# Optimization experiments

Hardware: AMD Instinct MI355X
Metric: run time of the kernel (lower is better)

## Reference

```python
import jax, jax.numpy as jnp
import numpy as np

ANGULAR = 5
N_LAYERS = 3
H = 384
W = 384
N = 1
RANK = 4
C = 3


def make_filters(angular, n_layers, h, w):
    """Replicates the buffer built in multilayer.__init__: shape [n_layers, angular^2, h, w, 2]."""
    x = np.linspace(-1.0, 1.0, w)
    y = np.linspace(-1.0, 1.0, h)
    xv, yv = np.meshgrid(x, y)
    default_flow = np.stack([xv, yv], axis=-1)  # [h, w, 2]
    disp = np.zeros((angular ** 2, h, w, 2))
    a = 0
    for k in range(-angular // 2 + 1, angular // 2 + 1):
        for l in range(-angular // 2 + 1, angular // 2 + 1):
            disp[a, :, :, 0] = (-1.0 / w) * l
            disp[a, :, :, 1] = (-1.0 / h) * k
            a += 1
    layers = np.stack([disp * c for c in range(-n_layers // 2 + 1, n_layers // 2 + 1)], 0)
    layers += default_flow[None, None, ...]
    return jnp.asarray(layers, dtype=jnp.float32)


def setup_inputs() -> dict:
    key = jax.random.key(0)
    layers = jax.random.normal(key, (N, N_LAYERS, RANK, C, H, W), dtype=jnp.float32)
    filters = make_filters(ANGULAR, N_LAYERS, H, W)
    return {"layers": layers, "filters": filters}


def _warp(img, grid):
    """Bilinear grid_sample, padding_mode='border', align_corners=True.
    img: [N, H, W, C] channel-last; grid: [H, W, 2] normalized coords in [-1, 1].
    Returns [N, H, W, C]."""
    h, w = img.shape[1], img.shape[2]
    # unnormalize with align_corners=True, then border-clamp the coordinate
    x = jnp.clip((grid[..., 0] + 1.0) * 0.5 * (w - 1), 0.0, w - 1.0)
    y = jnp.clip((grid[..., 1] + 1.0) * 0.5 * (h - 1), 0.0, h - 1.0)
    x0 = jnp.floor(x)
    y0 = jnp.floor(y)
    wx = (x - x0)[..., None]  # [H, W, 1]
    wy = (y - y0)[..., None]
    x0i = x0.astype(jnp.int32)
    y0i = y0.astype(jnp.int32)
    x1i = jnp.minimum(x0i + 1, w - 1)
    y1i = jnp.minimum(y0i + 1, h - 1)
    v00 = img[:, y0i, x0i]  # [N, H, W, C]
    v01 = img[:, y0i, x1i]
    v10 = img[:, y1i, x0i]
    v11 = img[:, y1i, x1i]
    top = v00 + wx * (v01 - v00)
    bot = v10 + wx * (v11 - v10)
    return top + wy * (bot - top)


def _forward(layers, filters):
    n, num_layers, rank, c, h, w = layers.shape
    a2 = filters.shape[1]
    # channel-last images per layer: [N, L, H, W, R*C]
    imgs = layers.reshape(n, num_layers, rank * c, h, w).transpose(0, 1, 3, 4, 2)
    warp_views = jax.vmap(_warp, in_axes=(None, 0))  # map over a^2 grids
    prod = warp_views(imgs[:, 0], filters[0])  # [a2, N, H, W, R*C]
    for l in range(1, num_layers):
        prod = prod * warp_views(imgs[:, l], filters[l])
    prod = prod.reshape(a2, n, h, w, rank, c)
    out = prod.mean(axis=4)  # reduce_mean over rank -> [a2, N, H, W, C]
    return out.transpose(1, 0, 4, 2, 3)  # [N, a2, C, H, W]


def reference(layers, filters):
    return _forward(layers, filters)
```

## Files before the change

kernel.cpp:

```cpp
#include <hip/hip_runtime.h>

#define H   384
#define W   384
#define HW  (H*W)
#define BLK 192

__device__ __forceinline__ float uread(float x) {
    return __int_as_float(__builtin_amdgcn_readfirstlane(__float_as_int(x)));
}

#define MKTAP(g_, pos_, t0, t1, t2)                                       \
    { float x_  = fminf(fmaxf(((g_) + 1.0f) * 0.5f * 383.0f, 0.0f), 383.0f); \
      float x0f = floorf(x_);                                             \
      float wx_ = x_ - x0f;                                               \
      int   dX  = (int)x0f - (pos_) + 1;                                  \
      t0 = dX ? 0.0f       : 1.0f - wx_;                                  \
      t1 = dX ? 1.0f - wx_ : wx_;                                         \
      t2 = dX ? wx_        : 0.0f; }

__global__ __launch_bounds__(BLK, 2) void multilayer_acc(
    const float* __restrict__ layers, float* __restrict__ out)
{
    const int lane = threadIdx.x & 63;
    const int c    = threadIdx.x >> 6;
    const int cu   = __builtin_amdgcn_readfirstlane(c);
    const int b    = (blockIdx.x & 7) * 288 + (blockIdx.x >> 3);
    const int i    = b / 6;
    const int j    = (b - i * 6) * 64 + lane;

    const double stepd = 2.0 / 383.0;
    const double flowx = (double)j * stepd - 1.0;
    const double flowy = (double)i * stepd - 1.0;

    float ax0[5][3], ax1[3];
#pragma unroll
    for (int v = 0; v < 5; ++v) {
        const double d = ((-1.0 / 384.0) * (double)(v - 2)) * (-1.0);
        const float  g = (float)(d + flowx);
        MKTAP(g, j, ax0[v][0], ax0[v][1], ax0[v][2])
    }
    { const float g = (float)flowx; MKTAP(g, j, ax1[0], ax1[1], ax1[2]) }

    float ay0[5][3], ay1[3];
#pragma unroll
    for (int v = 0; v < 5; ++v) {
        const double d = ((-1.0 / 384.0) * (double)(v - 2)) * (-1.0);
        const float  g = (float)(d + flowy);
        float t0, t1, t2;
        MKTAP(g, i, t0, t1, t2)
        ay0[v][0] = uread(t0); ay0[v][1] = uread(t1); ay0[v][2] = uread(t2);
    }
    {
        const float g = (float)flowy;
        float t0, t1, t2;
        MKTAP(g, i, t0, t1, t2)
        ay1[0] = uread(0.25f * t0); ay1[1] = uread(0.25f * t1); ay1[2] = uread(0.25f * t2);
    }

    const int jm = max(j - 1, 0), jp = min(j + 1, W - 1);
    const int im = max(i - 1, 0), ip = min(i + 1, H - 1);
    const int r0 = im * W, r1 = i * W, r2 = ip * W;
    const int voff[9] = { (r0 + jm) * 4, (r0 + j) * 4, (r0 + jp) * 4,
                          (r1 + jm) * 4, (r1 + j) * 4, (r1 + jp) * 4,
                          (r2 + jm) * 4, (r2 + j) * 4, (r2 + jp) * 4 };

    const char* base = (const char*)layers + (size_t)cu * (HW * 4);

    float acc[25];
#pragma unroll
    for (int a = 0; a < 25; ++a) acc[a] = 0.0f;

#define LOADR(r_, N0, N1, N2)                                             \
    { const char* p_ = base + (size_t)(r_) * (3 * HW * 4);                \
      _Pragma("unroll")                                                   \
      for (int t = 0; t < 9; ++t) {                                       \
          N0[t] = *(const float*)(p_ + voff[t]);                          \
          N1[t] = *(const float*)(p_ + (size_t)(12 * HW * 4) + voff[t]);  \
          N2[t] = *(const float*)(p_ + (size_t)(24 * HW * 4) + voff[t]);  \
      } }

#define COMPR(N0, N1, N2)                                                 \
    { float hy0 = ax1[0]*N1[0] + ax1[1]*N1[1] + ax1[2]*N1[2];             \
      float hy1 = ax1[0]*N1[3] + ax1[1]*N1[4] + ax1[2]*N1[5];             \
      float hy2 = ax1[0]*N1[6] + ax1[1]*N1[7] + ax1[2]*N1[8];             \
      const float v1 = ay1[0]*hy0 + ay1[1]*hy1 + ay1[2]*hy2;              \
      _Pragma("unroll")                                                   \
      for (int al = 0; al < 5; ++al) {                                    \
          float h0[3], h2[3];                                             \
          _Pragma("unroll")                                               \
          for (int dy = 0; dy < 3; ++dy) {                                \
              h0[dy] = (ax0[al][0]*N0[dy*3] + ax0[al][1]*N0[dy*3+1]       \
                        + ax0[al][2]*N0[dy*3+2]) * v1;                    \
              h2[dy] =  ax0[4-al][0]*N2[dy*3] + ax0[4-al][1]*N2[dy*3+1]   \
                        + ax0[4-al][2]*N2[dy*3+2];                        \
          }                                                               \
          _Pragma("unroll")                                               \
          for (int ak = 0; ak < 5; ++ak) {                                \
              const float s0 = ay0[ak][0]*h0[0] + ay0[ak][1]*h0[1]        \
                               + ay0[ak][2]*h0[2];                        \
              const float s2 = ay0[4-ak][0]*h2[0] + ay0[4-ak][1]*h2[1]    \
                               + ay0[4-ak][2]*h2[2];                      \
              acc[ak*5+al] = fmaf(s0, s2, acc[ak*5+al]);                  \
          } } }

    float Xa[9], Ya[9], Za[9], Xb[9], Yb[9], Zb[9], Xc[9], Yc[9], Zc[9];
    LOADR(0, Xa, Ya, Za)
    LOADR(1, Xb, Yb, Zb)
    LOADR(2, Xc, Yc, Zc)
    COMPR(Xa, Ya, Za)
    LOADR(3, Xa, Ya, Za)
    COMPR(Xb, Yb, Zb)
    COMPR(Xc, Yc, Zc)
    COMPR(Xa, Ya, Za)
#undef LOADR
#undef COMPR

    const size_t ob = (size_t)cu * HW + (size_t)i * W + j;
#pragma unroll
    for (int ak = 0; ak < 5; ++ak)
#pragma unroll
        for (int al = 0; al < 5; ++al)
            __builtin_nontemporal_store(acc[ak * 5 + al],
                out + (size_t)(ak * 5 + al) * (3 * HW) + ob);
}

extern "C" void kernel_launch(void* const* d_in, const int* in_sizes, int n_in,
                              void* d_out, int out_size, void* d_ws, size_t ws_size,
                              hipStream_t stream) {
    const float* layers = (const float*)d_in[0];
    float* out = (float*)d_out;

    const int n_blocks = HW / 64;
    multilayer_acc<<<n_blocks, BLK, 0, stream>>>(layers, out);
}
```

Before: 150.8 us.

## Accumulate per-row outer products over rank, apply vertical weights once at end

Reassociates the rank reduction: each rank adds 3x3 outer products of the horizontally interpolated rows of layers 0 and 2 into per-column matrices. The vertical bilinear weights are applied only once in the epilogue. This cuts per-rank ALU work substantially and drops one triple of load buffers, which shortens the prefetch depth. The cost is more accumulator registers, less load/compute overlap, and a slightly different float summation order.

Result: no change. 149.6 us (-0.8%).

```diff
diff --git a/kernel.cpp b/kernel.cpp
--- a/kernel.cpp
+++ b/kernel.cpp
@@ -18,7 +18,7 @@
       t1 = dX ? 1.0f - wx_ : wx_;                                         \
       t2 = dX ? wx_        : 0.0f; }
 
-__global__ __launch_bounds__(BLK, 2) void multilayer_acc(
+__global__ __launch_bounds__(BLK, 2) void multilayer_m2(
     const float* __restrict__ layers, float* __restrict__ out)
 {
     const int lane = threadIdx.x & 63;
@@ -66,9 +66,7 @@
 
     const char* base = (const char*)layers + (size_t)cu * (HW * 4);
 
-    float acc[25];
-#pragma unroll
-    for (int a = 0; a < 25; ++a) acc[a] = 0.0f;
+    float M[5][3][3] = {};
 
 #define LOADR(r_, N0, N1, N2)                                             \
     { const char* p_ = base + (size_t)(r_) * (3 * HW * 4);                \
@@ -79,7 +77,7 @@
           N2[t] = *(const float*)(p_ + (size_t)(24 * HW * 4) + voff[t]);  \
       } }
 
-#define COMPR(N0, N1, N2)                                                 \
+#define COMPM(N0, N1, N2)                                                 \
     { float hy0 = ax1[0]*N1[0] + ax1[1]*N1[1] + ax1[2]*N1[2];             \
       float hy1 = ax1[0]*N1[3] + ax1[1]*N1[4] + ax1[2]*N1[5];             \
       float hy2 = ax1[0]*N1[6] + ax1[1]*N1[7] + ax1[2]*N1[8];             \
@@ -95,33 +93,38 @@
                         + ax0[4-al][2]*N2[dy*3+2];                        \
           }                                                               \
           _Pragma("unroll")                                               \
-          for (int ak = 0; ak < 5; ++ak) {                                \
-              const float s0 = ay0[ak][0]*h0[0] + ay0[ak][1]*h0[1]        \
-                               + ay0[ak][2]*h0[2];                        \
-              const float s2 = ay0[4-ak][0]*h2[0] + ay0[4-ak][1]*h2[1]    \
-                               + ay0[4-ak][2]*h2[2];                      \
-              acc[ak*5+al] = fmaf(s0, s2, acc[ak*5+al]);                  \
-          } } }
+          for (int p = 0; p < 3; ++p)                                     \
+              _Pragma("unroll")                                           \
+              for (int q = 0; q < 3; ++q)                                 \
+                  M[al][p][q] = fmaf(h0[p], h2[q], M[al][p][q]);          \
+      } }
 
-    float Xa[9], Ya[9], Za[9], Xb[9], Yb[9], Zb[9], Xc[9], Yc[9], Zc[9];
+    float Xa[9], Ya[9], Za[9], Xb[9], Yb[9], Zb[9];
     LOADR(0, Xa, Ya, Za)
     LOADR(1, Xb, Yb, Zb)
-    LOADR(2, Xc, Yc, Zc)
-    COMPR(Xa, Ya, Za)
-    LOADR(3, Xa, Ya, Za)
-    COMPR(Xb, Yb, Zb)
-    COMPR(Xc, Yc, Zc)
-    COMPR(Xa, Ya, Za)
+    COMPM(Xa, Ya, Za)
+    LOADR(2, Xa, Ya, Za)
+    COMPM(Xb, Yb, Zb)
+    LOADR(3, Xb, Yb, Zb)
+    COMPM(Xa, Ya, Za)
+    COMPM(Xb, Yb, Zb)
 #undef LOADR
-#undef COMPR
+#undef COMPM
 
     const size_t ob = (size_t)cu * HW + (size_t)i * W + j;
 #pragma unroll
-    for (int ak = 0; ak < 5; ++ak)
+    for (int ak = 0; ak < 5; ++ak) {
+        const float q0 = ay0[4 - ak][0], q1 = ay0[4 - ak][1], q2 = ay0[4 - ak][2];
+        const float l0 = ay0[ak][0],     l1 = ay0[ak][1],     l2 = ay0[ak][2];
 #pragma unroll
-        for (int al = 0; al < 5; ++al)
-            __builtin_nontemporal_store(acc[ak * 5 + al],
-                out + (size_t)(ak * 5 + al) * (3 * HW) + ob);
+        for (int al = 0; al < 5; ++al) {
+            const float t0 = M[al][0][0] * q0 + M[al][0][1] * q1 + M[al][0][2] * q2;
+            const float t1 = M[al][1][0] * q0 + M[al][1][1] * q1 + M[al][1][2] * q2;
+            const float t2 = M[al][2][0] * q0 + M[al][2][1] * q1 + M[al][2][2] * q2;
+            const float s  = l0 * t0 + l1 * t1 + l2 * t2;
+            __builtin_nontemporal_store(s, out + (size_t)(ak * 5 + al) * (3 * HW) + ob);
+        }
+    }
 }
 
 extern "C" void kernel_launch(void* const* d_in, const int* in_sizes, int n_in,
@@ -131,5 +134,5 @@
     float* out = (float*)d_out;
 
     const int n_blocks = HW / 64;
-    multilayer_acc<<<n_blocks, BLK, 0, stream>>>(layers, out);
+    multilayer_m2<<<n_blocks, BLK, 0, stream>>>(layers, out);
 }
```
